# Kernel optimization log

Hardware: AMD Instinct MI355X
Metric: run time of the kernel (lower is better)

Reference implementation:

```python
import jax, jax.numpy as jnp
import numpy as np
from jax import lax

IN_CH = 512
OUT_CH = 512
KERNEL = 3
STYLE_DIM = 512
BATCH = 8
HW = 64
EPS = 1e-08
LR_MUL = 1.0


def setup_inputs() -> dict:
    key = jax.random.key(0)
    k1, k2, k3, k4 = jax.random.split(key, 4)
    x = jax.random.normal(k1, (BATCH, IN_CH, HW, HW), dtype=jnp.float32)
    style = jax.random.normal(k2, (BATCH, STYLE_DIM), dtype=jnp.float32)
    weight = jax.random.normal(k3, (1, OUT_CH, IN_CH, KERNEL, KERNEL), dtype=jnp.float32)
    mod_weight = jax.random.normal(k4, (IN_CH, STYLE_DIM), dtype=jnp.float32)
    mod_bias = jnp.ones((IN_CH,), dtype=jnp.float32)  # bias_init=1
    return {"x": x, "style": style, "weight": weight,
            "mod_weight": mod_weight, "mod_bias": mod_bias}


def reference(x, style, weight, mod_weight, mod_bias):
    batch, in_ch, h, w_dim = x.shape
    conv_scale = 1.0 / np.sqrt(in_ch * KERNEL * KERNEL)
    lin_scale = 1.0 / np.sqrt(STYLE_DIM) * LR_MUL

    # EqualizedLinear modulation: style -> per-channel scale, shape (B, in_ch)
    s = style @ (mod_weight * lin_scale).T + mod_bias * LR_MUL

    # Modulate: (B, out, in, k, k)
    w = conv_scale * weight * s[:, None, :, None, None]
    # Demodulate
    demod = lax.rsqrt(jnp.sum(w * w, axis=(2, 3, 4)) + EPS)  # (B, out)
    w = w * demod[:, :, None, None, None]

    pad = KERNEL // 2

    def conv_one(xi, wi):
        # xi: (in, H, W), wi: (out, in, k, k)
        return lax.conv_general_dilated(
            xi[None], wi, window_strides=(1, 1),
            padding=[(pad, pad), (pad, pad)],
            dimension_numbers=("NCHW", "OIHW", "NCHW"))[0]

    out = jax.vmap(conv_one)(x, w)  # (B, out, H, W)
    return out
```

## Files before the change

kernel.cpp:

```cpp
#include <hip/hip_runtime.h>
#include <hip/hip_bf16.h>
#include <cstdint>

#define IN_CH 512
#define OUT_CH 512
#define STYLE_DIM 512
#define BATCH 8
#define HW 64

typedef __bf16 bf16x8 __attribute__((ext_vector_type(8)));
typedef float f32x16 __attribute__((ext_vector_type(16)));

__device__ __forceinline__ void gload_lds16(const void* g, void* l) {
  __builtin_amdgcn_global_load_lds(
      (const __attribute__((address_space(1))) unsigned int*)g,
      (__attribute__((address_space(3))) unsigned int*)l,
      16, 0, 0);
}

#define WAITV(N) asm volatile("s_waitcnt vmcnt(" #N ")" ::: "memory")
#define BARRIER() do { asm volatile("" ::: "memory"); __builtin_amdgcn_s_barrier(); \
                       asm volatile("" ::: "memory"); } while (0)

__global__ void k_style(const float* __restrict__ style, const float* __restrict__ modw,
                        const float* __restrict__ modb, float* __restrict__ s_out) {
  __shared__ float st[BATCH * STYLE_DIM];
  const int tid = threadIdx.x;
  for (int i = tid; i < BATCH * STYLE_DIM; i += 256) st[i] = style[i];
  __syncthreads();
  const int ic = blockIdx.x * 4 + (tid >> 6);
  const int l = tid & 63;
  const float* mr = modw + (size_t)ic * STYLE_DIM + l * 8;
  float m[8];
  #pragma unroll
  for (int j = 0; j < 8; ++j) m[j] = mr[j];
  float accs[8];
  #pragma unroll
  for (int b = 0; b < 8; ++b) {
    const float* sb = st + b * STYLE_DIM + l * 8;
    float a = 0.f;
    #pragma unroll
    for (int j = 0; j < 8; ++j) a += m[j] * sb[j];
    accs[b] = a;
  }
  #pragma unroll
  for (int off = 32; off; off >>= 1) {
    #pragma unroll
    for (int b = 0; b < 8; ++b) accs[b] += __shfl_down(accs[b], off, 64);
  }
  if (l == 0) {
    #pragma unroll
    for (int b = 0; b < 8; ++b)
      s_out[b * IN_CH + ic] = accs[b] * 0.04419417382415922f + modb[ic];
  }
}

__global__ void k_wprep(const float* __restrict__ w, float* __restrict__ wsq,
                        __bf16* __restrict__ wb) {
  const int idx = blockIdx.x * 256 + threadIdx.x;
  const int oc = idx >> 9, ic = idx & 511;
  const float* p = w + ((size_t)oc * IN_CH + ic) * 9;
  float sum = 0.f;
  #pragma unroll
  for (int t = 0; t < 9; ++t) {
    float v = p[t];
    sum += v * v;
    wb[((size_t)(t * OUT_CH) + oc) * IN_CH + ic] = (__bf16)v;
  }
  wsq[oc * IN_CH + ic] = sum;
}

__global__ void k_demod(const float* __restrict__ s, const float* __restrict__ wsq,
                        float* __restrict__ scale) {
  const int oc = blockIdx.x;
  const int l = threadIdx.x;
  const float* wr = wsq + (size_t)oc * IN_CH + l * 8;
  float w8[8];
  #pragma unroll
  for (int j = 0; j < 8; ++j) w8[j] = wr[j];
  #pragma unroll
  for (int b = 0; b < 8; ++b) {
    const float* sb = s + b * IN_CH + l * 8;
    float acc = 0.f;
    #pragma unroll
    for (int j = 0; j < 8; ++j) { float sv = sb[j]; acc += sv * sv * w8[j]; }
    #pragma unroll
    for (int off = 32; off; off >>= 1) acc += __shfl_down(acc, off, 64);
    if (l == 0)
      scale[b * OUT_CH + oc] =
          rsqrtf(acc * (1.0f / 4608.0f) + 1e-8f) * 0.014731391274719732f;
  }
}

__global__ void k_xprep(const float* __restrict__ x, const float* __restrict__ s,
                        __bf16* __restrict__ xg) {
  const int b = blockIdx.x >> 6, y = blockIdx.x & 63;
  const int w = threadIdx.x >> 6, lane = threadIdx.x & 63;
  const float* sr = s + b * IN_CH;
  #pragma unroll
  for (int it = 0; it < 8; ++it) {
    const int ug = it * 8 + w;
    bf16x8 pk;
    #pragma unroll
    for (int j = 0; j < 8; ++j) {
      const int ic = ug * 8 + j;
      pk[j] = (__bf16)(x[(((size_t)(b * IN_CH) + ic) * HW + y) * HW + lane] * sr[ic]);
    }
    *(bf16x8*)(xg + ((((size_t)(b * 64 + ug) * HW + y) * HW + lane) * 8)) = pk;
  }
}

__global__ __launch_bounds__(512, 2) void k_conv(
    const __bf16* __restrict__ Wg,
    const __bf16* __restrict__ Xg,
    const float* __restrict__ scale,
    const __bf16* __restrict__ zpg,
    float* __restrict__ out)
{
  __shared__ __attribute__((aligned(16))) __bf16 Xs[3584 * 8];
  __shared__ __attribute__((aligned(16))) __bf16 Wl[3][2048 * 8];

  const int tid = threadIdx.x;
  const int lane = tid & 63;
  const int wid = tid >> 6;
  const int wm = wid >> 2;
  const int wn = wid & 3;
  const int ln31 = lane & 31;
  const int laneK = lane >> 5;
  const int kord = wid & 3;

  const int bid0 = blockIdx.x;
  const int bid = (bid0 & 7) * 32 + (bid0 >> 3);
  const int octile = bid & 1;
  const int ptile = (bid >> 1) & 15;
  const int b = bid >> 5;
  const int oc0 = octile * 256;
  const int r0 = ptile * 4;

  auto stage_w = [&](int chunkv, int tapv, int bsel) {
    #pragma unroll
    for (int i = 0; i < 4; ++i) {
      const int u = i * 512 + tid;
      const int j = u >> 4, p = u & 15;
      const int row = 2 * j + (p & 1);
      const int s = ((p >> 1) - j) & 7;
      gload_lds16(Wg + (((size_t)(tapv * OUT_CH) + oc0 + row) * IN_CH + chunkv * 64 + s * 8),
                  (void*)((char*)Wl[bsel] + u * 16));
    }
  };
  auto stage_x = [&](int chunkv) {
    #pragma unroll
    for (int i = 0; i < 7; ++i) {
      const int u = i * 512 + tid;
      const int j = u >> 4, p = u & 15;
      const int R = 2 * j + (p & 1);
      const int s = ((p >> 1) - j) & 7;
      const int xrow = (int)((unsigned)R / 66u);
      const int col = R - 66 * xrow;
      const int y = r0 - 1 + xrow;
      const bool ok = (col >= 1) & (col <= 64) & (y >= 0) & (y < HW);
      const __bf16* src = ok
          ? Xg + ((((size_t)(b * 64 + chunkv * 8 + s) * HW + y) * HW + (col - 1)) * 8)
          : zpg;
      gload_lds16(src, (void*)((char*)Xs + u * 16));
    }
  };

  stage_x(0);
  stage_w(0, 0, 0);
  stage_w(0, 1, 1);

  const int keyA = ln31 + 2 * laneK + 4 * kord;
  int aoff8[4];
  #pragma unroll
  for (int ks = 0; ks < 4; ++ks) aoff8[ks] = ((keyA + 4 * ks) & 15) * 8;
  const __bf16* __restrict__ ab0 = Wl[0] + (64 * wm + (ln31 >> 1)) * 128;
  const __bf16* __restrict__ ab1 = Wl[1] + (64 * wm + (ln31 >> 1)) * 128;
  const __bf16* __restrict__ ab2 = Wl[2] + (64 * wm + (ln31 >> 1)) * 128;
  const int RB = wn * 66 + ln31;
  const int kB0 = RB + 2 * laneK + 4 * kord;

  f32x16 acc[4][2] = {};

#define TAPBODY(T) { \
    if ((T) == 8 && c == 7) { WAITV(0); } else { WAITV(4); } \
    BARRIER(); \
    const __bf16* __restrict__ abase = ((T) % 3 == 0) ? ab0 : ((T) % 3 == 1) ? ab1 : ab2; \
    const int Rt = RB + ((T) / 3) * 66 + ((T) % 3); \
    const int kBt = kB0 + ((T) / 3) * 66 + ((T) % 3); \
    const __bf16* __restrict__ xbase = Xs + (Rt >> 1) * 128; \
    _Pragma("unroll") \
    for (int ks = 0; ks < 4; ++ks) { \
      const int bp = ((kBt + 4 * ks) & 15) * 8; \
      bf16x8 av[4], bv[2]; \
      _Pragma("unroll") \
      for (int mf = 0; mf < 4; ++mf) av[mf] = *(const bf16x8*)(abase + mf * 2048 + aoff8[ks]); \
      bv[0] = *(const bf16x8*)(xbase + bp); \
      bv[1] = *(const bf16x8*)(xbase + 2048 + bp); \
      __builtin_amdgcn_s_setprio(1); \
      _Pragma("unroll") \
      for (int mf = 0; mf < 4; ++mf) { \
        acc[mf][0] = __builtin_amdgcn_mfma_f32_32x32x16_bf16(av[mf], bv[0], acc[mf][0], 0, 0, 0); \
        acc[mf][1] = __builtin_amdgcn_mfma_f32_32x32x16_bf16(av[mf], bv[1], acc[mf][1], 0, 0, 0); \
      } \
      __builtin_amdgcn_s_setprio(0); \
    } \
    if ((T) == 8) { \
      if (c < 7) { BARRIER(); stage_x(c + 1); stage_w(c + 1, 1, 1); } \
    } else if ((T) <= 6) { \
      stage_w(c, (T) + 2, ((T) + 2) % 3); \
    } else {  \
      if (c < 7) stage_w(c + 1, 0, 0); \
    } \
  }

  #pragma unroll 1
  for (int c = 0; c < 8; ++c) {
    TAPBODY(0) TAPBODY(1) TAPBODY(2)
    TAPBODY(3) TAPBODY(4) TAPBODY(5)
    TAPBODY(6) TAPBODY(7) TAPBODY(8)
  }

  const int y = r0 + wn;
  #pragma unroll
  for (int mf = 0; mf < 4; ++mf) {
    #pragma unroll
    for (int reg = 0; reg < 16; ++reg) {
      const int rowid = (reg & 3) + 8 * (reg >> 2) + 4 * laneK;
      const int oc = oc0 + 128 * wm + 32 * mf + rowid;
      const float sc = scale[b * OUT_CH + oc];
      float* op = out + (((size_t)(b * OUT_CH + oc) * HW + y) * HW) + ln31;
      op[0] = acc[mf][0][reg] * sc;
      op[32] = acc[mf][1][reg] * sc;
    }
  }
}

extern "C" void kernel_launch(void* const* d_in, const int* in_sizes, int n_in,
                              void* d_out, int out_size, void* d_ws, size_t ws_size,
                              hipStream_t stream) {
  const float* x      = (const float*)d_in[0];
  const float* style  = (const float*)d_in[1];
  const float* weight = (const float*)d_in[2];
  const float* modw   = (const float*)d_in[3];
  const float* modb   = (const float*)d_in[4];
  float* out = (float*)d_out;

  char* ws = (char*)d_ws;
  float*  s_buf = (float*)(ws + 0);
  float*  scale = (float*)(ws + 16384);
  __bf16* zpg   = (__bf16*)(ws + 32768);
  float*  wsq   = (float*)(ws + 36864);
  __bf16* wb    = (__bf16*)(ws + 36864 + 1048576);
  __bf16* xg    = (__bf16*)(ws + 36864 + 1048576 + 9 * OUT_CH * IN_CH * 2);

  hipMemsetAsync(zpg, 0, 4096, stream);
  k_style<<<128, 256, 0, stream>>>(style, modw, modb, s_buf);
  k_wprep<<<1024, 256, 0, stream>>>(weight, wsq, wb);
  k_demod<<<512, 64, 0, stream>>>(s_buf, wsq, scale);
  k_xprep<<<BATCH * HW, 512, 0, stream>>>(x, s_buf, xg);
  k_conv<<<256, 512, 0, stream>>>(wb, xg, scale, zpg, out);
}
```

Measured before the change: 200.1 us.

## Pre-swizzle weight and input tensors in global memory to match LDS tiles

The weight and activation prep kernels now write bf16 data directly in the swizzled, LDS-ready order, including zero padding columns for the input rows. The conv kernel's staging then becomes contiguous 16-byte copies with no per-element index arithmetic, division by 66, or scattered global addresses. B-operand LDS offsets are precomputed per tap column into registers. This is meant to cut address computation and improve global load coalescing in the main loop. The cost is more register use, a changed swizzle pattern that must stay bank-conflict free, and a larger padded input buffer.

```diff
diff --git a/kernel.cpp b/kernel.cpp
--- a/kernel.cpp
+++ b/kernel.cpp
@@ -56,16 +56,20 @@
 }
 
 __global__ void k_wprep(const float* __restrict__ w, float* __restrict__ wsq,
-                        __bf16* __restrict__ wb) {
+                        __bf16* __restrict__ wgp) {
   const int idx = blockIdx.x * 256 + threadIdx.x;
   const int oc = idx >> 9, ic = idx & 511;
-  const float* p = w + ((size_t)oc * IN_CH + ic) * 9;
+  const int octile = oc >> 8, R = oc & 255, j = R >> 1;
+  const int chunk = ic >> 6, sslot = (ic >> 3) & 7, e = ic & 7;
+  const int p = 2 * ((sslot + j) & 7) + (R & 1);
+  const int u = j * 16 + p;
+  const float* pw = w + ((size_t)oc * IN_CH + ic) * 9;
   float sum = 0.f;
   #pragma unroll
   for (int t = 0; t < 9; ++t) {
-    float v = p[t];
+    float v = pw[t];
     sum += v * v;
-    wb[((size_t)(t * OUT_CH) + oc) * IN_CH + ic] = (__bf16)v;
+    wgp[((size_t)((t * 8 + chunk) * 2 + octile) * 2048 + u) * 8 + e] = (__bf16)v;
   }
   wsq[oc * IN_CH + ic] = sum;
 }
@@ -93,26 +97,40 @@
 }
 
 __global__ void k_xprep(const float* __restrict__ x, const float* __restrict__ s,
-                        __bf16* __restrict__ xg) {
+                        __bf16* __restrict__ xgp) {
   const int b = blockIdx.x >> 6, y = blockIdx.x & 63;
-  const int w = threadIdx.x >> 6, lane = threadIdx.x & 63;
+  const int t = threadIdx.x;
+  const int xcol = t & 63;
+  const int g0 = t >> 6;
   const float* sr = s + b * IN_CH;
-  #pragma unroll
-  for (int it = 0; it < 8; ++it) {
-    const int ug = it * 8 + w;
+  const size_t rowbase = ((size_t)(b * 64 + y)) * 8 * 528;
+  #pragma unroll
+  for (int i = 0; i < 8; ++i) {
+    const int g = i * 8 + g0;
     bf16x8 pk;
     #pragma unroll
-    for (int j = 0; j < 8; ++j) {
-      const int ic = ug * 8 + j;
-      pk[j] = (__bf16)(x[(((size_t)(b * IN_CH) + ic) * HW + y) * HW + lane] * sr[ic]);
-    }
-    *(bf16x8*)(xg + ((((size_t)(b * 64 + ug) * HW + y) * HW + lane) * 8)) = pk;
+    for (int e = 0; e < 8; ++e) {
+      const int ic = g * 8 + e;
+      pk[e] = (__bf16)(x[(((size_t)(b * IN_CH) + ic) * HW + y) * HW + xcol] * sr[ic]);
+    }
+    const int col = xcol + 1, c = col >> 1;
+    const int p = 2 * (((g & 7) + c) & 7) + (col & 1);
+    const int u = c * 16 + p;
+    *(bf16x8*)(xgp + (rowbase + (size_t)(g >> 3) * 528 + u) * 8) = pk;
+  }
+  if (t < 128) {
+    const int col = (t & 1) * 65, g = t >> 1;
+    const int c = col >> 1;
+    const int p = 2 * (((g & 7) + c) & 7) + (col & 1);
+    const int u = c * 16 + p;
+    bf16x8 z = {};
+    *(bf16x8*)(xgp + (rowbase + (size_t)(g >> 3) * 528 + u) * 8) = z;
   }
 }
 
 __global__ __launch_bounds__(512, 2) void k_conv(
-    const __bf16* __restrict__ Wg,
-    const __bf16* __restrict__ Xg,
+    const __bf16* __restrict__ Wgp,
+    const __bf16* __restrict__ Xgp,
     const float* __restrict__ scale,
     const __bf16* __restrict__ zpg,
     float* __restrict__ out)
@@ -127,40 +145,33 @@
   const int wn = wid & 3;
   const int ln31 = lane & 31;
   const int laneK = lane >> 5;
-  const int kord = wid & 3;
 
   const int bid0 = blockIdx.x;
   const int bid = (bid0 & 7) * 32 + (bid0 >> 3);
   const int octile = bid & 1;
   const int ptile = (bid >> 1) & 15;
   const int b = bid >> 5;
+  const int r0 = ptile * 4;
   const int oc0 = octile * 256;
-  const int r0 = ptile * 4;
 
   auto stage_w = [&](int chunkv, int tapv, int bsel) {
+    const __bf16* base = Wgp + (size_t)((tapv * 8 + chunkv) * 2 + octile) * (2048 * 8);
     #pragma unroll
     for (int i = 0; i < 4; ++i) {
       const int u = i * 512 + tid;
-      const int j = u >> 4, p = u & 15;
-      const int row = 2 * j + (p & 1);
-      const int s = ((p >> 1) - j) & 7;
-      gload_lds16(Wg + (((size_t)(tapv * OUT_CH) + oc0 + row) * IN_CH + chunkv * 64 + s * 8),
-                  (void*)((char*)Wl[bsel] + u * 16));
+      gload_lds16(base + (size_t)u * 8, (void*)((char*)Wl[bsel] + u * 16));
     }
   };
   auto stage_x = [&](int chunkv) {
     #pragma unroll
     for (int i = 0; i < 7; ++i) {
-      const int u = i * 512 + tid;
-      const int j = u >> 4, p = u & 15;
-      const int R = 2 * j + (p & 1);
-      const int s = ((p >> 1) - j) & 7;
-      const int xrow = (int)((unsigned)R / 66u);
-      const int col = R - 66 * xrow;
-      const int y = r0 - 1 + xrow;
-      const bool ok = (col >= 1) & (col <= 64) & (y >= 0) & (y < HW);
+      const unsigned u = i * 512 + tid;
+      const unsigned row = u / 528u;
+      const unsigned rr = u - row * 528u;
+      const int y = r0 - 1 + (int)row;
+      const bool ok = (u < 3168u) & (y >= 0) & (y < HW);
       const __bf16* src = ok
-          ? Xg + ((((size_t)(b * 64 + chunkv * 8 + s) * HW + y) * HW + (col - 1)) * 8)
+          ? Xgp + (((size_t)(b * 64 + y) * 8 + chunkv) * 528 + rr) * 8
           : zpg;
       gload_lds16(src, (void*)((char*)Xs + u * 16));
     }
@@ -170,15 +181,22 @@
   stage_w(0, 0, 0);
   stage_w(0, 1, 1);
 
-  const int keyA = ln31 + 2 * laneK + 4 * kord;
   int aoff8[4];
   #pragma unroll
-  for (int ks = 0; ks < 4; ++ks) aoff8[ks] = ((keyA + 4 * ks) & 15) * 8;
+  for (int ks = 0; ks < 4; ++ks) aoff8[ks] = ((ln31 + 4 * ks + 2 * laneK) & 15) * 8;
+  int bele[3][4];
+  #pragma unroll
+  for (int dxi = 0; dxi < 3; ++dxi) {
+    const int col = ln31 + dxi, c = col >> 1;
+    #pragma unroll
+    for (int ks = 0; ks < 4; ++ks) {
+      const int pos = (col & 1) + 2 * ((2 * ks + laneK + c) & 7);
+      bele[dxi][ks] = c * 128 + pos * 8;
+    }
+  }
   const __bf16* __restrict__ ab0 = Wl[0] + (64 * wm + (ln31 >> 1)) * 128;
   const __bf16* __restrict__ ab1 = Wl[1] + (64 * wm + (ln31 >> 1)) * 128;
   const __bf16* __restrict__ ab2 = Wl[2] + (64 * wm + (ln31 >> 1)) * 128;
-  const int RB = wn * 66 + ln31;
-  const int kB0 = RB + 2 * laneK + 4 * kord;
 
   f32x16 acc[4][2] = {};
 
@@ -186,17 +204,16 @@
     if ((T) == 8 && c == 7) { WAITV(0); } else { WAITV(4); } \
     BARRIER(); \
     const __bf16* __restrict__ abase = ((T) % 3 == 0) ? ab0 : ((T) % 3 == 1) ? ab1 : ab2; \
-    const int Rt = RB + ((T) / 3) * 66 + ((T) % 3); \
-    const int kBt = kB0 + ((T) / 3) * 66 + ((T) % 3); \
-    const __bf16* __restrict__ xbase = Xs + (Rt >> 1) * 128; \
+    const __bf16* __restrict__ xbase = Xs + (wn + (T) / 3) * (33 * 128); \
     _Pragma("unroll") \
     for (int ks = 0; ks < 4; ++ks) { \
-      const int bp = ((kBt + 4 * ks) & 15) * 8; \
+      const int ael = aoff8[ks]; \
+      const int bel = bele[(T) % 3][ks]; \
       bf16x8 av[4], bv[2]; \
       _Pragma("unroll") \
-      for (int mf = 0; mf < 4; ++mf) av[mf] = *(const bf16x8*)(abase + mf * 2048 + aoff8[ks]); \
-      bv[0] = *(const bf16x8*)(xbase + bp); \
-      bv[1] = *(const bf16x8*)(xbase + 2048 + bp); \
+      for (int mf = 0; mf < 4; ++mf) av[mf] = *(const bf16x8*)(abase + mf * 2048 + ael); \
+      bv[0] = *(const bf16x8*)(xbase + bel); \
+      bv[1] = *(const bf16x8*)(xbase + 2048 + bel); \
       __builtin_amdgcn_s_setprio(1); \
       _Pragma("unroll") \
       for (int mf = 0; mf < 4; ++mf) { \
@@ -250,14 +267,14 @@
   float*  s_buf = (float*)(ws + 0);
   float*  scale = (float*)(ws + 16384);
   __bf16* zpg   = (__bf16*)(ws + 32768);
-  float*  wsq   = (float*)(ws + 36864);
-  __bf16* wb    = (__bf16*)(ws + 36864 + 1048576);
-  __bf16* xg    = (__bf16*)(ws + 36864 + 1048576 + 9 * OUT_CH * IN_CH * 2);
-
-  hipMemsetAsync(zpg, 0, 4096, stream);
+  float*  wsq   = (float*)(ws + 49152);
+  __bf16* wgp   = (__bf16*)(ws + 49152 + 1048576);
+  __bf16* xgp   = (__bf16*)(ws + 49152 + 1048576 + 9 * 8 * 2 * 2048 * 8 * 2);
+
+  hipMemsetAsync(zpg, 0, 16384, stream);
   k_style<<<128, 256, 0, stream>>>(style, modw, modb, s_buf);
-  k_wprep<<<1024, 256, 0, stream>>>(weight, wsq, wb);
+  k_wprep<<<1024, 256, 0, stream>>>(weight, wsq, wgp);
   k_demod<<<512, 64, 0, stream>>>(s_buf, wsq, scale);
-  k_xprep<<<BATCH * HW, 512, 0, stream>>>(x, s_buf, xg);
-  k_conv<<<256, 512, 0, stream>>>(wb, xg, scale, zpg, out);
-}
+  k_xprep<<<BATCH * HW, 512, 0, stream>>>(x, s_buf, xgp);
+  k_conv<<<256, 512, 0, stream>>>(wgp, xgp, scale, zpg, out);
+}
```

After: 167.2 us. 16.5% less time.
